# Performance work log

Measured on AMD Instinct MI355X. Metric: run time of the kernel, lower is better.

## Reference

```python
import jax, jax.numpy as jnp
import numpy as np
from functools import partial

TOP_K = 2
LN_EPS = 1e-5


def setup_inputs() -> dict:
    key = jax.random.key(0)
    ks = jax.random.split(key, 4)
    B, T, H, F, E = 2, 2048, 1024, 4096, 8
    hidden_states = jax.random.normal(ks[0], (B, T, H), dtype=jnp.float32)
    # Router weights: original inits to zeros; use small random so routing is non-degenerate.
    router_w = jax.random.normal(ks[1], (E, H), dtype=jnp.float32) * 0.02
    router_b = jnp.zeros((E,), dtype=jnp.float32)
    W1 = jax.random.normal(ks[2], (E, H, F), dtype=jnp.float32) * (1.0 / np.sqrt(H))
    b1 = jnp.zeros((E, F), dtype=jnp.float32)
    W2 = jax.random.normal(ks[3], (E, F, H), dtype=jnp.float32) * (1.0 / np.sqrt(F))
    b2 = jnp.zeros((E, H), dtype=jnp.float32)
    ln_gamma = jnp.ones((H,), dtype=jnp.float32)
    ln_beta = jnp.zeros((H,), dtype=jnp.float32)
    return {"hidden_states": hidden_states, "router_w": router_w, "router_b": router_b,
            "W1": W1, "b1": b1, "W2": W2, "b2": b2,
            "ln_gamma": ln_gamma, "ln_beta": ln_beta}


def _layer_norm(x, gamma, beta):
    mu = jnp.mean(x, axis=-1, keepdims=True)
    var = jnp.var(x, axis=-1, keepdims=True)
    return (x - mu) * jax.lax.rsqrt(var + LN_EPS) * gamma + beta


def _moe_forward(hidden_states, router_w, router_b, W1, b1, W2, b2, ln_gamma, ln_beta):
    B, T, H = hidden_states.shape
    E = router_w.shape[0]
    N = B * T
    x = hidden_states.reshape(N, H)
    # Router (jitter=0.0, eval mode): logits [N, E]
    logits = x @ router_w.T + router_b
    topk_vals, topk_idx = jax.lax.top_k(logits, TOP_K)        # [N, K]
    topk_w = jax.nn.softmax(topk_vals, axis=-1)               # [N, K]
    # Scatter top-k weights into a dense combine matrix [N, E] (zeros elsewhere).
    probs = jnp.zeros((N, E), dtype=x.dtype).at[jnp.arange(N)[:, None], topk_idx].set(topk_w)
    # Per-expert FFN via scan over the (small, fixed) expert axis; each step is one
    # big GEMM over all tokens weighted by that expert's combine prob (0 for
    # tokens not routed to it) — same math as gather/MLP/scatter with no capacity drop.
    def body(acc, params_e):
        Wa, ba, Wb, bb, pe = params_e          # pe: [N]
        h = jax.nn.gelu(x @ Wa + ba, approximate=False)   # [N, F]
        y = h @ Wb + bb                                    # [N, H]
        return acc + y * pe[:, None], None
    out, _ = jax.lax.scan(body, jnp.zeros_like(x), (W1, b1, W2, b2, probs.T))
    out = out.reshape(B, T, H)
    return _layer_norm(out + hidden_states, ln_gamma, ln_beta)


def reference(hidden_states, router_w, router_b, W1, b1, W2, b2, ln_gamma, ln_beta):
    return _moe_forward(hidden_states, router_w, router_b, W1, b1, W2, b2, ln_gamma, ln_beta)
```

## Files before the change

kernel.cpp:

```cpp
#include <hip/hip_runtime.h>
#include <hip/hip_bf16.h>


typedef unsigned short u16;
typedef unsigned int u32;
typedef __attribute__((ext_vector_type(4))) float f32x4;
typedef __attribute__((ext_vector_type(8))) short s16x8;
typedef __attribute__((ext_vector_type(4))) unsigned short u16x4;
typedef __attribute__((ext_vector_type(8))) unsigned short u16x8;

#define GLD16(gp, lp) __builtin_amdgcn_global_load_lds( \
    (const __attribute__((address_space(1))) void*)(gp), \
    (__attribute__((address_space(3))) void*)(lp), 16, 0, 0)

__device__ __forceinline__ u16 f2bf(float f) {
    union { float f; u32 u; } v; v.f = f;
    u32 u = v.u;
    return (u16)((u + 0x7fffu + ((u >> 16) & 1u)) >> 16);
}
__device__ __forceinline__ float bf2f(u16 h) {
    union { u32 u; float f; } v; v.u = ((u32)h) << 16; return v.f;
}

__device__ __forceinline__ float gelu_f(float v) {
    const float u = v * (0.7978845608f + 0.0356774081f * v * v);
    const float t = __expf(-2.0f * u);
    return v * __builtin_amdgcn_rcpf(1.0f + t);
}

__global__ void k_init(int* cc) { if (threadIdx.x < 16) cc[threadIdx.x] = 0; }

__global__ __launch_bounds__(256) void k_pre(
    const float* __restrict__ x, const float* __restrict__ rw, const float* __restrict__ rb,
    u16* __restrict__ xb, int* __restrict__ eidx, float* __restrict__ wgt, int* __restrict__ counts,
    const float* __restrict__ W1, u16* __restrict__ W1t,
    const float* __restrict__ W2, u16* __restrict__ W2t)
{
    __shared__ u16 tl[128 * 128];
    const int id = blockIdx.x;
    const int tid = threadIdx.x;

    if (id >= 1024) {
        const float* s; u16* d; int K, N, k0, n0;
        if (id < 3072) {
            const int id2 = id - 1024;
            const int e = id2 >> 8, rem = id2 & 255;
            K = 1024; N = 4096;
            k0 = (rem >> 5) * 128; n0 = (rem & 31) * 128;
            s = W1 + (size_t)e * 1024 * 4096; d = W1t + (size_t)e * 1024 * 4096;
        } else {
            const int id3 = id - 3072;
            const int e = id3 >> 8, rem = id3 & 255;
            K = 4096; N = 1024;
            k0 = (rem >> 3) * 128; n0 = (rem & 7) * 128;
            s = W2 + (size_t)e * 4096 * 1024; d = W2t + (size_t)e * 1024 * 4096;
        }

        const int nq = (tid & 31) * 4;
        const int kb = (tid >> 5) * 4;
        #pragma unroll
        for (int iter = 0; iter < 4; ++iter) {
            const int k = iter * 32 + kb;
            const float4 r0 = *(const float4*)(s + (size_t)(k0 + k    ) * N + n0 + nq);
            const float4 r1 = *(const float4*)(s + (size_t)(k0 + k + 1) * N + n0 + nq);
            const float4 r2 = *(const float4*)(s + (size_t)(k0 + k + 2) * N + n0 + nq);
            const float4 r3 = *(const float4*)(s + (size_t)(k0 + k + 3) * N + n0 + nq);
            const int c16 = k >> 3, half = (k >> 2) & 1;
            const float rrr[4][4] = {{r0.x,r1.x,r2.x,r3.x},{r0.y,r1.y,r2.y,r3.y},
                                     {r0.z,r1.z,r2.z,r3.z},{r0.w,r1.w,r2.w,r3.w}};
            #pragma unroll
            for (int i = 0; i < 4; ++i) {
                const int n = nq + i;
                const int c16s = c16 ^ (n & 15) ^ (((n >> 4) & 3) << 2);
                u16x4 p;
                p[0] = f2bf(rrr[i][0]); p[1] = f2bf(rrr[i][1]);
                p[2] = f2bf(rrr[i][2]); p[3] = f2bf(rrr[i][3]);
                *(u16x4*)(&tl[n * 128 + c16s * 8 + half * 4]) = p;
            }
        }
        __syncthreads();
        #pragma unroll
        for (int rr2 = 0; rr2 < 4; ++rr2) {
            const int n = rr2 * 32 + (tid >> 3);
            #pragma unroll
            for (int ci = 0; ci < 2; ++ci) {
                const int c16 = ci * 8 + (tid & 7);
                const int c16s = c16 ^ (n & 15) ^ (((n >> 4) & 3) << 2);
                const u16x8 v = *(const u16x8*)(&tl[n * 128 + c16s * 8]);
                *(u16x8*)(d + (size_t)(n0 + n) * K + k0 + c16 * 8) = v;
            }
        }
        return;
    }

    const int wav = tid >> 6, lane = tid & 63;
    const int t = id * 4 + wav;
    const float* xt = x + (size_t)t * 1024;
    float acc[8] = {0.f,0.f,0.f,0.f,0.f,0.f,0.f,0.f};
    #pragma unroll
    for (int c = 0; c < 4; c++) {
        const int base = c * 256 + lane * 4;
        const float4 xv = *(const float4*)(xt + base);
        ushort4 pk;
        pk.x = f2bf(xv.x); pk.y = f2bf(xv.y); pk.z = f2bf(xv.z); pk.w = f2bf(xv.w);
        *(ushort4*)(xb + (size_t)t * 1024 + base) = pk;
        #pragma unroll
        for (int e = 0; e < 8; e++) {
            const float4 wv = *(const float4*)(rw + e * 1024 + base);
            acc[e] += xv.x * wv.x + xv.y * wv.y + xv.z * wv.z + xv.w * wv.w;
        }
    }
    #pragma unroll
    for (int e = 0; e < 8; e++) {
        #pragma unroll
        for (int s = 32; s; s >>= 1) acc[e] += __shfl_xor(acc[e], s);
    }
    if (lane == 0) {
        float v0 = -3e38f, v1 = -3e38f; int i0 = 0, i1 = 0;
        #pragma unroll
        for (int e = 0; e < 8; e++) {
            const float l = acc[e] + rb[e];
            if (l > v0) { v1 = v0; i1 = i0; v0 = l; i0 = e; }
            else if (l > v1) { v1 = l; i1 = e; }
        }
        const float w0 = 1.0f / (1.0f + expf(v1 - v0));
        eidx[2 * t] = i0; eidx[2 * t + 1] = i1;
        wgt[2 * t] = w0; wgt[2 * t + 1] = 1.0f - w0;
        atomicAdd(&counts[i0], 1); atomicAdd(&counts[i1], 1);
    }
}

__global__ __launch_bounds__(256) void k_place2(
    const int* __restrict__ eidx, const int* __restrict__ counts, int* __restrict__ cursors,
    int* __restrict__ offsets, int* __restrict__ rows, int* __restrict__ pos_of)
{
    int base[8];
    int s = 0;
    #pragma unroll
    for (int e = 0; e < 8; e++) { base[e] = s; s += counts[e]; }
    if (blockIdx.x == 0 && threadIdx.x == 0) {
        #pragma unroll
        for (int e = 0; e < 8; e++) offsets[e] = base[e];
        offsets[8] = s;
    }
    const int a = blockIdx.x * 256 + threadIdx.x;
    const int e = eidx[a];
    const int pos = base[e] + atomicAdd(&cursors[e], 1);
    rows[pos] = a >> 1;
    pos_of[a] = pos;
}

#define STAGE_T(b, k0) { \
    char* ad = (char*)At + (b) * 8192 + wav * 1024; \
    char* bd = (char*)Bt + (b) * 8192 + wav * 1024; \
    GLD16(a_src0 + (k0), ad); \
    GLD16(a_src1 + (k0), ad + 4096); \
    GLD16(b_src0 + (k0), bd); \
    GLD16(b_src1 + (k0), bd + 4096); }

#define COMPUTE_T(b) { \
    const u16* Abp = Ab + (b) * 4096; \
    const u16* Bbp = Bb + (b) * 4096; \
    s16x8 af[4], bfr[4]; \
    _Pragma("unroll") \
    for (int i = 0; i < 4; i++) { \
        af[i]  = *(const s16x8*)(Abp + i * 512); \
        bfr[i] = *(const s16x8*)(Bbp + i * 512); \
    } \
    __builtin_amdgcn_s_setprio(1); \
    _Pragma("unroll") \
    for (int mi = 0; mi < 4; mi++) \
        _Pragma("unroll") \
        for (int ni = 0; ni < 4; ni++) \
            acc[mi][ni] = __builtin_amdgcn_mfma_f32_16x16x32_bf16(af[mi], bfr[ni], acc[mi][ni], 0, 0, 0); \
    __builtin_amdgcn_s_setprio(0); }

#define VMCNT4 asm volatile("s_waitcnt vmcnt(4)" ::: "memory")
#define VMCNT0 asm volatile("s_waitcnt vmcnt(0)" ::: "memory")
#define BAR __builtin_amdgcn_s_barrier()

__global__ __launch_bounds__(256, 4) void k_gemm1(
    const u16* __restrict__ xb, const u16* __restrict__ W1t, const float* __restrict__ b1,
    u16* __restrict__ hbuf, const int* __restrict__ rows, const int* __restrict__ offsets)
{
    const int fid = blockIdx.x;
    const int swz = (fid & 7) * 1024 + (fid >> 3);
    const int y = swz & 31, xx = (swz >> 5) & 31, e = swz >> 10;

    const int off = offsets[e], cnt = offsets[e + 1] - off;
    const int row0 = y * 128;
    if (row0 >= cnt) return;
    const int n0 = xx * 128;
    const int tid = threadIdx.x;
    const int lane = tid & 63, wav = tid >> 6, lane15 = lane & 15;

    __shared__ u16 At[2][128][32];
    __shared__ u16 Bt[2][128][32];

    const int ar0 = tid >> 2;
    const int cl8 = (((tid & 3) ^ ((tid >> 3) & 3))) * 8;
    const int t0 = rows[off + min(row0 + ar0, cnt - 1)];
    const int t1 = rows[off + min(row0 + ar0 + 64, cnt - 1)];
    const u16* a_src0 = xb + (size_t)t0 * 1024 + cl8;
    const u16* a_src1 = xb + (size_t)t1 * 1024 + cl8;
    const u16* b_src0 = W1t + ((size_t)e * 4096 + n0 + ar0) * 1024 + cl8;
    const u16* b_src1 = b_src0 + (size_t)64 * 1024;

    f32x4 acc[4][4] = {};
    const int wr = wav >> 1, wc = wav & 1;
    const int koff = ((lane >> 4) ^ ((lane >> 1) & 3)) * 8;
    const u16* Ab = &At[0][wr * 64 + lane15][koff];
    const u16* Bb = &Bt[0][wc * 64 + lane15][koff];

    STAGE_T(0, 0);
    int b = 0;
    for (int k0 = 32; k0 < 1024; k0 += 32) {
        STAGE_T(b ^ 1, k0);
        VMCNT4;
        BAR;
        COMPUTE_T(b);
        BAR;
        b ^= 1;
    }
    VMCNT0;
    BAR;
    COMPUTE_T(b);

    const int rb4 = (lane >> 4) * 4;
    const int colbase = n0 + wc * 64 + lane15;
    float bias[4];
    #pragma unroll
    for (int ni = 0; ni < 4; ni++) bias[ni] = b1[e * 4096 + colbase + ni * 16];
    #pragma unroll
    for (int mi = 0; mi < 4; mi++) {
        #pragma unroll
        for (int j = 0; j < 4; j++) {
            const int lrow = wr * 64 + mi * 16 + rb4 + j;
            if (row0 + lrow < cnt) {
                const size_t gr = (size_t)(off + row0 + lrow);
                #pragma unroll
                for (int ni = 0; ni < 4; ni++) {
                    const float v = acc[mi][ni][j] + bias[ni];
                    hbuf[gr * 4096 + colbase + ni * 16] = f2bf(gelu_f(v));
                }
            }
        }
    }
}

__global__ __launch_bounds__(256, 4) void k_gemm2(
    const u16* __restrict__ hbuf, const u16* __restrict__ W2t, const float* __restrict__ b2,
    u16* __restrict__ yb, const int* __restrict__ offsets)
{
    const int fid = blockIdx.x;
    const int swz = (fid & 7) * 1024 + (fid >> 3);
    const int y = swz & 31, xx = (swz >> 5) & 7, z = swz >> 8;
    const int e = z >> 2, kq = z & 3;

    const int off = offsets[e], cnt = offsets[e + 1] - off;
    const int row0 = y * 128;
    if (row0 >= cnt) return;
    const int n0 = xx * 128;
    const int tid = threadIdx.x;
    const int lane = tid & 63, wav = tid >> 6, lane15 = lane & 15;
    const int kbase = kq * 1024;

    __shared__ u16 At[2][128][32];
    __shared__ u16 Bt[2][128][32];

    const int ar0 = tid >> 2;
    const int cl8 = (((tid & 3) ^ ((tid >> 3) & 3))) * 8;
    const u16* a_src0 = hbuf + (size_t)(off + min(row0 + ar0, cnt - 1)) * 4096 + kbase + cl8;
    const u16* a_src1 = hbuf + (size_t)(off + min(row0 + ar0 + 64, cnt - 1)) * 4096 + kbase + cl8;
    const u16* b_src0 = W2t + ((size_t)e * 1024 + n0 + ar0) * 4096 + kbase + cl8;
    const u16* b_src1 = b_src0 + (size_t)64 * 4096;

    f32x4 acc[4][4] = {};
    const int wr = wav >> 1, wc = wav & 1;
    const int koff = ((lane >> 4) ^ ((lane >> 1) & 3)) * 8;
    const u16* Ab = &At[0][wr * 64 + lane15][koff];
    const u16* Bb = &Bt[0][wc * 64 + lane15][koff];

    STAGE_T(0, 0);
    int b = 0;
    for (int k0 = 32; k0 < 1024; k0 += 32) {
        STAGE_T(b ^ 1, k0);
        VMCNT4;
        BAR;
        COMPUTE_T(b);
        BAR;
        b ^= 1;
    }
    VMCNT0;
    BAR;
    COMPUTE_T(b);

    u16* yy = yb + (size_t)kq * 8192 * 1024;
    const int rb4 = (lane >> 4) * 4;
    const int colbase = n0 + wc * 64 + lane15;
    float bias[4];
    #pragma unroll
    for (int ni = 0; ni < 4; ni++) bias[ni] = (kq == 0) ? b2[e * 1024 + colbase + ni * 16] : 0.f;
    #pragma unroll
    for (int mi = 0; mi < 4; mi++) {
        #pragma unroll
        for (int j = 0; j < 4; j++) {
            const int lrow = wr * 64 + mi * 16 + rb4 + j;
            if (row0 + lrow < cnt) {
                const size_t gr = (size_t)(off + row0 + lrow);
                #pragma unroll
                for (int ni = 0; ni < 4; ni++)
                    yy[gr * 1024 + colbase + ni * 16] = f2bf(acc[mi][ni][j] + bias[ni]);
            }
        }
    }
}

__global__ __launch_bounds__(256) void k_combine(
    const float* __restrict__ x, const u16* __restrict__ yb,
    const int* __restrict__ pos_of, const float* __restrict__ wgt,
    const float* __restrict__ gamma, const float* __restrict__ beta,
    float* __restrict__ out)
{
    const int t = blockIdx.x;
    const int tid = threadIdx.x;
    const int p0 = pos_of[2 * t], p1 = pos_of[2 * t + 1];
    const float w0 = wgt[2 * t], w1 = wgt[2 * t + 1];
    const int j4 = tid * 4;
    const float4 xv = *(const float4*)(x + (size_t)t * 1024 + j4);
    float s0[4] = {0.f, 0.f, 0.f, 0.f};
    float s1[4] = {0.f, 0.f, 0.f, 0.f};
    #pragma unroll
    for (int kq = 0; kq < 4; kq++) {
        const u16* ybq = yb + (size_t)kq * 8192 * 1024;
        const ushort4 u0 = *(const ushort4*)(ybq + (size_t)p0 * 1024 + j4);
        const ushort4 u1 = *(const ushort4*)(ybq + (size_t)p1 * 1024 + j4);
        s0[0] += bf2f(u0.x); s0[1] += bf2f(u0.y); s0[2] += bf2f(u0.z); s0[3] += bf2f(u0.w);
        s1[0] += bf2f(u1.x); s1[1] += bf2f(u1.y); s1[2] += bf2f(u1.z); s1[3] += bf2f(u1.w);
    }
    float a0 = xv.x + w0 * s0[0] + w1 * s1[0];
    float a1 = xv.y + w0 * s0[1] + w1 * s1[1];
    float a2 = xv.z + w0 * s0[2] + w1 * s1[2];
    float a3 = xv.w + w0 * s0[3] + w1 * s1[3];
    float s = a0 + a1 + a2 + a3;
    float q = a0 * a0 + a1 * a1 + a2 * a2 + a3 * a3;
    #pragma unroll
    for (int o = 32; o; o >>= 1) { s += __shfl_xor(s, o); q += __shfl_xor(q, o); }
    __shared__ float ls[4], lq[4];
    const int wav = tid >> 6, lane = tid & 63;
    if (lane == 0) { ls[wav] = s; lq[wav] = q; }
    __syncthreads();
    s = ls[0] + ls[1] + ls[2] + ls[3];
    q = lq[0] + lq[1] + lq[2] + lq[3];
    const float mu = s * (1.0f / 1024.0f);
    const float var = q * (1.0f / 1024.0f) - mu * mu;
    const float rs = rsqrtf(var + 1e-5f);
    const float4 g = *(const float4*)(gamma + j4);
    const float4 b = *(const float4*)(beta + j4);
    float4 o4;
    o4.x = (a0 - mu) * rs * g.x + b.x;
    o4.y = (a1 - mu) * rs * g.y + b.y;
    o4.z = (a2 - mu) * rs * g.z + b.z;
    o4.w = (a3 - mu) * rs * g.w + b.w;
    *(float4*)(out + (size_t)t * 1024 + j4) = o4;
}

extern "C" void kernel_launch(void* const* d_in, const int* in_sizes, int n_in,
                              void* d_out, int out_size, void* d_ws, size_t ws_size,
                              hipStream_t stream) {
    const float* x     = (const float*)d_in[0];
    const float* rw    = (const float*)d_in[1];
    const float* rb    = (const float*)d_in[2];
    const float* W1    = (const float*)d_in[3];
    const float* b1    = (const float*)d_in[4];
    const float* W2    = (const float*)d_in[5];
    const float* b2    = (const float*)d_in[6];
    const float* gamma = (const float*)d_in[7];
    const float* beta  = (const float*)d_in[8];
    float* out = (float*)d_out;

    char* p = (char*)d_ws;
    auto alloc = [&](size_t bytes) { char* r = p; p += (bytes + 255) & ~(size_t)255; return r; };
    int*   counts  = (int*)alloc(16 * sizeof(int));
    int*   cursors = counts + 8;
    int*   offsets = (int*)alloc(9 * sizeof(int));
    int*   eidx    = (int*)alloc(8192 * sizeof(int));
    float* wgt     = (float*)alloc(8192 * sizeof(float));
    int*   pos_of  = (int*)alloc(8192 * sizeof(int));
    int*   rows    = (int*)alloc(8192 * sizeof(int));
    u16*   xb      = (u16*)alloc((size_t)4096 * 1024 * 2);
    u16*   W1t     = (u16*)alloc((size_t)8 * 4096 * 1024 * 2);
    u16*   W2t     = (u16*)alloc((size_t)8 * 1024 * 4096 * 2);
    u16*   hbuf    = (u16*)alloc((size_t)8192 * 4096 * 2);
    u16* yb = W1t;

    hipLaunchKernelGGL(k_init, dim3(1), dim3(64), 0, stream, counts);
    hipLaunchKernelGGL(k_pre, dim3(5120), dim3(256), 0, stream,
                       x, rw, rb, xb, eidx, wgt, counts, W1, W1t, W2, W2t);
    hipLaunchKernelGGL(k_place2, dim3(32), dim3(256), 0, stream,
                       eidx, counts, cursors, offsets, rows, pos_of);
    hipLaunchKernelGGL(k_gemm1, dim3(8192), dim3(256), 0, stream, xb, W1t, b1, hbuf, rows, offsets);
    hipLaunchKernelGGL(k_gemm2, dim3(8192), dim3(256), 0, stream, hbuf, W2t, b2, yb, offsets);
    hipLaunchKernelGGL(k_combine, dim3(4096), dim3(256), 0, stream, x, yb, pos_of, wgt, gamma, beta, out);
}
```

Baseline: 423.4 us.

## Store transposed bf16 weights in K-tiled 32-wide panels for contiguous GEMM B loads

Changes the weight preprocessing so W1/W2 are written as [K/32][N][32] bf16 panels instead of row-major [N][K]. The transpose now stages a 32x512 tile through LDS and writes each output row as contiguous 64-byte chunks. Both expert GEMM kernels compute B-operand addresses with the new panel stride, so each k-step reads one contiguous 8KB block rather than 128 rows strided by K. This aims to make the weight transpose and the GEMM B-tile fetches more cache and DRAM friendly. The trade-off is that the LDS swizzle in the transpose is dropped, which may introduce bank conflicts.

```diff
diff --git a/kernel.cpp b/kernel.cpp
--- a/kernel.cpp
+++ b/kernel.cpp
@@ -30,65 +30,61 @@
 
 __global__ void k_init(int* cc) { if (threadIdx.x < 16) cc[threadIdx.x] = 0; }
 
+__device__ __forceinline__ void transp_tiled(
+    const float* __restrict__ s, u16* __restrict__ d, int K, int N,
+    int k0, int n0, int tid)
+{
+    __shared__ u16 tl[32 * 512];
+    const int w = tid >> 6, l = tid & 63;
+    #pragma unroll
+    for (int i = 0; i < 8; ++i) {
+        const int r = i * 4 + w;
+        #pragma unroll
+        for (int h = 0; h < 2; ++h) {
+            const int q = h * 64 + l;
+            const float4 v = *(const float4*)(s + (size_t)(k0 + r) * N + n0 + q * 4);
+            u16x4 p;
+            p[0] = f2bf(v.x); p[1] = f2bf(v.y); p[2] = f2bf(v.z); p[3] = f2bf(v.w);
+            *(u16x4*)(&tl[r * 512 + q * 4]) = p;
+        }
+    }
+    __syncthreads();
+    u16 rowA[32], rowB[32];
+    #pragma unroll
+    for (int k = 0; k < 32; ++k) {
+        const u32 v = *(const u32*)(&tl[k * 512 + tid * 2]);
+        rowA[k] = (u16)(v & 0xffffu);
+        rowB[k] = (u16)(v >> 16);
+    }
+    u16* dp = d + ((size_t)(k0 >> 5) * N + n0 + tid * 2) * 32;
+    #pragma unroll
+    for (int c = 0; c < 4; ++c) *(u16x8*)(dp + c * 8)      = *(u16x8*)(&rowA[c * 8]);
+    #pragma unroll
+    for (int c = 0; c < 4; ++c) *(u16x8*)(dp + 32 + c * 8) = *(u16x8*)(&rowB[c * 8]);
+}
+
 __global__ __launch_bounds__(256) void k_pre(
     const float* __restrict__ x, const float* __restrict__ rw, const float* __restrict__ rb,
     u16* __restrict__ xb, int* __restrict__ eidx, float* __restrict__ wgt, int* __restrict__ counts,
     const float* __restrict__ W1, u16* __restrict__ W1t,
     const float* __restrict__ W2, u16* __restrict__ W2t)
 {
-    __shared__ u16 tl[128 * 128];
     const int id = blockIdx.x;
     const int tid = threadIdx.x;
 
     if (id >= 1024) {
-        const float* s; u16* d; int K, N, k0, n0;
         if (id < 3072) {
             const int id2 = id - 1024;
             const int e = id2 >> 8, rem = id2 & 255;
-            K = 1024; N = 4096;
-            k0 = (rem >> 5) * 128; n0 = (rem & 31) * 128;
-            s = W1 + (size_t)e * 1024 * 4096; d = W1t + (size_t)e * 1024 * 4096;
+            const int kt = rem >> 3, nq = rem & 7;
+            transp_tiled(W1 + (size_t)e * 1024 * 4096, W1t + (size_t)e * 1024 * 4096,
+                         1024, 4096, kt * 32, nq * 512, tid);
         } else {
             const int id3 = id - 3072;
             const int e = id3 >> 8, rem = id3 & 255;
-            K = 4096; N = 1024;
-            k0 = (rem >> 3) * 128; n0 = (rem & 7) * 128;
-            s = W2 + (size_t)e * 4096 * 1024; d = W2t + (size_t)e * 1024 * 4096;
-        }
-
-        const int nq = (tid & 31) * 4;
-        const int kb = (tid >> 5) * 4;
-        #pragma unroll
-        for (int iter = 0; iter < 4; ++iter) {
-            const int k = iter * 32 + kb;
-            const float4 r0 = *(const float4*)(s + (size_t)(k0 + k    ) * N + n0 + nq);
-            const float4 r1 = *(const float4*)(s + (size_t)(k0 + k + 1) * N + n0 + nq);
-            const float4 r2 = *(const float4*)(s + (size_t)(k0 + k + 2) * N + n0 + nq);
-            const float4 r3 = *(const float4*)(s + (size_t)(k0 + k + 3) * N + n0 + nq);
-            const int c16 = k >> 3, half = (k >> 2) & 1;
-            const float rrr[4][4] = {{r0.x,r1.x,r2.x,r3.x},{r0.y,r1.y,r2.y,r3.y},
-                                     {r0.z,r1.z,r2.z,r3.z},{r0.w,r1.w,r2.w,r3.w}};
-            #pragma unroll
-            for (int i = 0; i < 4; ++i) {
-                const int n = nq + i;
-                const int c16s = c16 ^ (n & 15) ^ (((n >> 4) & 3) << 2);
-                u16x4 p;
-                p[0] = f2bf(rrr[i][0]); p[1] = f2bf(rrr[i][1]);
-                p[2] = f2bf(rrr[i][2]); p[3] = f2bf(rrr[i][3]);
-                *(u16x4*)(&tl[n * 128 + c16s * 8 + half * 4]) = p;
-            }
-        }
-        __syncthreads();
-        #pragma unroll
-        for (int rr2 = 0; rr2 < 4; ++rr2) {
-            const int n = rr2 * 32 + (tid >> 3);
-            #pragma unroll
-            for (int ci = 0; ci < 2; ++ci) {
-                const int c16 = ci * 8 + (tid & 7);
-                const int c16s = c16 ^ (n & 15) ^ (((n >> 4) & 3) << 2);
-                const u16x8 v = *(const u16x8*)(&tl[n * 128 + c16s * 8]);
-                *(u16x8*)(d + (size_t)(n0 + n) * K + k0 + c16 * 8) = v;
-            }
+            const int kt = rem >> 1, nq = rem & 1;
+            transp_tiled(W2 + (size_t)e * 4096 * 1024, W2t + (size_t)e * 1024 * 4096,
+                         4096, 1024, kt * 32, nq * 512, tid);
         }
         return;
     }
@@ -150,13 +146,13 @@
     pos_of[a] = pos;
 }
 
-#define STAGE_T(b, k0) { \
+#define STAGE_T(b, aoff, boff) { \
     char* ad = (char*)At + (b) * 8192 + wav * 1024; \
     char* bd = (char*)Bt + (b) * 8192 + wav * 1024; \
-    GLD16(a_src0 + (k0), ad); \
-    GLD16(a_src1 + (k0), ad + 4096); \
-    GLD16(b_src0 + (k0), bd); \
-    GLD16(b_src1 + (k0), bd + 4096); }
+    GLD16(a_src0 + (aoff), ad); \
+    GLD16(a_src1 + (aoff), ad + 4096); \
+    GLD16(b_src0 + (boff), bd); \
+    GLD16(b_src1 + (boff), bd + 4096); }
 
 #define COMPUTE_T(b) { \
     const u16* Abp = Ab + (b) * 4096; \
@@ -203,8 +199,8 @@
     const int t1 = rows[off + min(row0 + ar0 + 64, cnt - 1)];
     const u16* a_src0 = xb + (size_t)t0 * 1024 + cl8;
     const u16* a_src1 = xb + (size_t)t1 * 1024 + cl8;
-    const u16* b_src0 = W1t + ((size_t)e * 4096 + n0 + ar0) * 1024 + cl8;
-    const u16* b_src1 = b_src0 + (size_t)64 * 1024;
+    const u16* b_src0 = W1t + (size_t)e * 4096 * 1024 + (size_t)(n0 + ar0) * 32 + cl8;
+    const u16* b_src1 = b_src0 + (size_t)64 * 32;
 
     f32x4 acc[4][4] = {};
     const int wr = wav >> 1, wc = wav & 1;
@@ -212,10 +208,10 @@
     const u16* Ab = &At[0][wr * 64 + lane15][koff];
     const u16* Bb = &Bt[0][wc * 64 + lane15][koff];
 
-    STAGE_T(0, 0);
+    STAGE_T(0, 0, 0);
     int b = 0;
     for (int k0 = 32; k0 < 1024; k0 += 32) {
-        STAGE_T(b ^ 1, k0);
+        STAGE_T(b ^ 1, k0, (size_t)k0 * 4096);
         VMCNT4;
         BAR;
         COMPUTE_T(b);
@@ -272,8 +268,8 @@
     const int cl8 = (((tid & 3) ^ ((tid >> 3) & 3))) * 8;
     const u16* a_src0 = hbuf + (size_t)(off + min(row0 + ar0, cnt - 1)) * 4096 + kbase + cl8;
     const u16* a_src1 = hbuf + (size_t)(off + min(row0 + ar0 + 64, cnt - 1)) * 4096 + kbase + cl8;
-    const u16* b_src0 = W2t + ((size_t)e * 1024 + n0 + ar0) * 4096 + kbase + cl8;
-    const u16* b_src1 = b_src0 + (size_t)64 * 4096;
+    const u16* b_src0 = W2t + (size_t)e * 1024 * 4096 + (size_t)(n0 + ar0) * 32 + cl8;
+    const u16* b_src1 = b_src0 + (size_t)64 * 32;
 
     f32x4 acc[4][4] = {};
     const int wr = wav >> 1, wc = wav & 1;
@@ -281,10 +277,10 @@
     const u16* Ab = &At[0][wr * 64 + lane15][koff];
     const u16* Bb = &Bt[0][wc * 64 + lane15][koff];
 
-    STAGE_T(0, 0);
+    STAGE_T(0, 0, (size_t)kbase * 1024);
     int b = 0;
     for (int k0 = 32; k0 < 1024; k0 += 32) {
-        STAGE_T(b ^ 1, k0);
+        STAGE_T(b ^ 1, k0, (size_t)(kbase + k0) * 1024);
         VMCNT4;
         BAR;
         COMPUTE_T(b);
```

Measured after the change: 438.9 us. +3.7%, slower.
